# Optimization experiments

Hardware: AMD Instinct MI355X
Metric: run time of the kernel (lower is better)

## Reference

```python
import jax, jax.numpy as jnp
import numpy as np

NUM_NODES = 100000
NUM_EDGES = 1600000
INPUT_DIM = 128
HIDDEN_DIM = 64
OUTPUT_DIM = 2
DROPOUT_P = 0.5


def setup_inputs() -> dict:
    key = jax.random.key(0)
    ks = jax.random.split(key, 6)
    x = jax.random.normal(ks[0], (NUM_NODES, INPUT_DIM), dtype=jnp.float32)
    edge_index = jax.random.randint(ks[1], (2, NUM_EDGES), 0, NUM_NODES, dtype=jnp.int64)
    W_conv = jax.random.normal(ks[2], (INPUT_DIM, HIDDEN_DIM), dtype=jnp.float32) * (1.0 / np.sqrt(INPUT_DIM))
    b_conv = jax.random.normal(ks[3], (HIDDEN_DIM,), dtype=jnp.float32) * 0.02
    W_lin = jax.random.normal(ks[4], (HIDDEN_DIM, OUTPUT_DIM), dtype=jnp.float32) * (1.0 / np.sqrt(HIDDEN_DIM))
    b_lin = jax.random.normal(ks[5], (OUTPUT_DIM,), dtype=jnp.float32) * 0.02
    return {"x": x, "edge_index": edge_index, "W_conv": W_conv, "b_conv": b_conv,
            "W_lin": W_lin, "b_lin": b_lin}


def _gcn_conv(x, edge_index, W, b):
    n = x.shape[0]
    # linear transform first (PyG GCNConv)
    h = x @ W  # [N, hidden]
    # add self-loops
    loop = jnp.arange(n, dtype=edge_index.dtype)
    row = jnp.concatenate([edge_index[0], loop])  # source
    col = jnp.concatenate([edge_index[1], loop])  # target
    # symmetric normalization deg^{-1/2} (degree counted on targets, incl. self-loops)
    deg = jax.ops.segment_sum(jnp.ones_like(col, dtype=h.dtype), col, num_segments=n)
    dinv = jnp.where(deg > 0, jax.lax.rsqrt(deg), 0.0)
    norm = dinv[row] * dinv[col]  # [E+N]
    # gather -> scale -> scatter-add
    msgs = h[row] * norm[:, None]  # [E+N, hidden]
    out = jax.ops.segment_sum(msgs, col, num_segments=n)
    return out + b


def reference(x, edge_index, W_conv, b_conv, W_lin, b_lin):
    h = _gcn_conv(x, edge_index, W_conv, b_conv)
    h = jax.nn.relu(h)
    # dropout p=0.5, training mode, deterministic key for reproducibility
    keep = jax.random.bernoulli(jax.random.key(42), 1.0 - DROPOUT_P, h.shape)
    h = jnp.where(keep, h / (1.0 - DROPOUT_P), 0.0)
    return h @ W_lin + b_lin
```

## Files before the change

### kernel.cpp

```cpp
#include <hip/hip_runtime.h>
#include <hip/hip_bf16.h>

#define N_NODES 100000
#define N_EDGES 1600000
#define IN_DIM 128
#define HID 64
#define NB ((N_NODES + 255) / 256)
#define EPB 4096
#define BUCKET_BLOCKS ((N_EDGES + EPB - 1) / EPB)
#define MAXPB 8192

__device__ __forceinline__ unsigned rotl32(unsigned x, unsigned r) {
    return (x << r) | (x >> (32u - r));
}

__device__ __forceinline__ void threefry2x32_k42(unsigned x0, unsigned x1,
                                                 unsigned& o0, unsigned& o1) {
    const unsigned ks0 = 0u;
    const unsigned ks1 = 42u;
    const unsigned ks2 = 0u ^ 42u ^ 0x1BD11BDAu;
    x0 += ks0; x1 += ks1;
    x0 += x1; x1 = rotl32(x1, 13); x1 ^= x0;
    x0 += x1; x1 = rotl32(x1, 15); x1 ^= x0;
    x0 += x1; x1 = rotl32(x1, 26); x1 ^= x0;
    x0 += x1; x1 = rotl32(x1, 6);  x1 ^= x0;
    x0 += ks1; x1 += ks2 + 1u;
    x0 += x1; x1 = rotl32(x1, 17); x1 ^= x0;
    x0 += x1; x1 = rotl32(x1, 29); x1 ^= x0;
    x0 += x1; x1 = rotl32(x1, 16); x1 ^= x0;
    x0 += x1; x1 = rotl32(x1, 24); x1 ^= x0;
    x0 += ks2; x1 += ks0 + 2u;
    x0 += x1; x1 = rotl32(x1, 13); x1 ^= x0;
    x0 += x1; x1 = rotl32(x1, 15); x1 ^= x0;
    x0 += x1; x1 = rotl32(x1, 26); x1 ^= x0;
    x0 += x1; x1 = rotl32(x1, 6);  x1 ^= x0;
    x0 += ks0; x1 += ks1 + 3u;
    x0 += x1; x1 = rotl32(x1, 17); x1 ^= x0;
    x0 += x1; x1 = rotl32(x1, 29); x1 ^= x0;
    x0 += x1; x1 = rotl32(x1, 16); x1 ^= x0;
    x0 += x1; x1 = rotl32(x1, 24); x1 ^= x0;
    x0 += ks1; x1 += ks2 + 4u;
    x0 += x1; x1 = rotl32(x1, 13); x1 ^= x0;
    x0 += x1; x1 = rotl32(x1, 15); x1 ^= x0;
    x0 += x1; x1 = rotl32(x1, 26); x1 ^= x0;
    x0 += x1; x1 = rotl32(x1, 6);  x1 ^= x0;
    x0 += ks2; x1 += ks0 + 5u;
    o0 = x0; o1 = x1;
}

__device__ __forceinline__ float bf2f(unsigned short u) {
    return __uint_as_float((unsigned)u << 16);
}
__device__ __forceinline__ float bf2f_lo(unsigned u) {
    return __uint_as_float(u << 16);
}
__device__ __forceinline__ float bf2f_hi(unsigned u) {
    return __uint_as_float(u & 0xffff0000u);
}

__global__ __launch_bounds__(512) void k_bucket(const int* __restrict__ src,
                                                const int* __restrict__ dst,
                                                int* __restrict__ bucketcnt,
                                                unsigned* __restrict__ gbuf) {
    __shared__ int cnt[512];
    __shared__ int off[512];
    __shared__ int cur[NB];
    __shared__ int gbase[NB];
    __shared__ unsigned buf[EPB];
    __shared__ unsigned short bkt[EPB];
    const int t = threadIdx.x;
    const int e0 = blockIdx.x * EPB;
    const int n = min(EPB, N_EDGES - e0);
    cnt[t] = 0;
    __syncthreads();
    unsigned myrec[EPB / 512];
    int myb[EPB / 512];
#pragma unroll
    for (int k = 0; k < EPB / 512; k++) {
        int e = e0 + k * 512 + t;
        if (e < N_EDGES) {
            int r = src[e];
            int c = dst[e];
            int b = c >> 8;
            myrec[k] = ((unsigned)(c & 255) << 17) | (unsigned)r;
            myb[k] = b;
            atomicAdd(&cnt[b], 1);
        } else {
            myb[k] = -1;
        }
    }
    __syncthreads();
    int own = cnt[t];
    for (int o = 1; o < 512; o <<= 1) {
        int v = (t >= o) ? cnt[t - o] : 0;
        __syncthreads();
        cnt[t] += v;
        __syncthreads();
    }
    off[t] = cnt[t] - own;
    if (t < NB) {
        cur[t] = off[t];
        gbase[t] = t * MAXPB + (own ? atomicAdd(&bucketcnt[t], own) : 0);
    }
    __syncthreads();
#pragma unroll
    for (int k = 0; k < EPB / 512; k++) {
        if (myb[k] >= 0) {
            int p = atomicAdd(&cur[myb[k]], 1);
            buf[p] = myrec[k];
            bkt[p] = (unsigned short)myb[k];
        }
    }
    __syncthreads();
    for (int j = t; j < n; j += 512) {
        int b = bkt[j];
        gbuf[gbase[b] + (j - off[b])] = buf[j];
    }
}

__global__ __launch_bounds__(512) void k_scanB(const int* __restrict__ bucketcnt,
                                               int* __restrict__ bucket_base) {
    __shared__ int s[512];
    int t = threadIdx.x;
    int own = (t < NB) ? bucketcnt[t] : 0;
    s[t] = own;
    __syncthreads();
    for (int o = 1; o < 512; o <<= 1) {
        int v = (t >= o) ? s[t - o] : 0;
        __syncthreads();
        s[t] += v;
        __syncthreads();
    }
    if (t < NB) bucket_base[t] = s[t] - own;
    if (t == 511) bucket_base[NB] = s[511];
}

__global__ __launch_bounds__(256) void k_csr2(const unsigned* __restrict__ gbuf,
                                              const int* __restrict__ bucketcnt,
                                              const int* __restrict__ bucket_base,
                                              int* __restrict__ row_start,
                                              float* __restrict__ dinv,
                                              int* __restrict__ srcs) {
    __shared__ unsigned lbuf[MAXPB];
    __shared__ int lcnt[256];
    __shared__ int pre[256];
    __shared__ int cur[256];
    const int b = blockIdx.x, t = threadIdx.x;
    const int n = bucketcnt[b];
    const unsigned* reg = gbuf + (size_t)b * MAXPB;
    lcnt[t] = 0;
    for (int j = t; j < n; j += 256) lbuf[j] = reg[j];
    __syncthreads();
    for (int j = t; j < n; j += 256) atomicAdd(&lcnt[lbuf[j] >> 17], 1);
    __syncthreads();
    int my = lcnt[t];
    pre[t] = my;
    __syncthreads();
    for (int o = 1; o < 256; o <<= 1) {
        int v = (t >= o) ? pre[t - o] : 0;
        __syncthreads();
        pre[t] += v;
        __syncthreads();
    }
    const int gb = bucket_base[b];
    int base = gb + pre[t] - my;
    cur[t] = base;
    const int c = b * 256 + t;
    if (c < N_NODES) {
        row_start[c] = base;
        dinv[c] = rsqrtf((float)(my + 1));
    }
    if (b == NB - 1 && t == 255) row_start[N_NODES] = gb + pre[255];
    __syncthreads();
    for (int j = t; j < n; j += 256) {
        unsigned rec = lbuf[j];
        int pos = atomicAdd(&cur[rec >> 17], 1);
        srcs[pos] = (int)(rec & 0x1FFFF);
    }
}

__global__ __launch_bounds__(256) void k_gemm(const float* __restrict__ x,
                                              const float* __restrict__ W,
                                              const float* __restrict__ dinv,
                                              unsigned short* __restrict__ gm) {
    __shared__ float Wl[IN_DIM * HID];
    __shared__ float xs[16][IN_DIM];
    const int t = threadIdx.x;
    const float4* W4 = (const float4*)W;
    for (int i = t; i < IN_DIM * HID / 4; i += 256) ((float4*)Wl)[i] = W4[i];
    const int base = blockIdx.x * 16;
    const float4* x4 = (const float4*)(x + (size_t)base * IN_DIM);
    for (int i = t; i < 16 * IN_DIM / 4; i += 256) ((float4*)xs)[i] = x4[i];
    __syncthreads();
    const int d = t & 63, g = t >> 6;
    float wreg[IN_DIM];
#pragma unroll
    for (int k = 0; k < IN_DIM; k++) wreg[k] = Wl[k * HID + d];
    float a0 = 0.f, a1 = 0.f, a2 = 0.f, a3 = 0.f;
#pragma unroll
    for (int k = 0; k < IN_DIM; k += 4) {
        float4 xv0 = *(const float4*)&xs[g][k];
        float4 xv1 = *(const float4*)&xs[g + 4][k];
        float4 xv2 = *(const float4*)&xs[g + 8][k];
        float4 xv3 = *(const float4*)&xs[g + 12][k];
        a0 += xv0.x * wreg[k] + xv0.y * wreg[k + 1] + xv0.z * wreg[k + 2] + xv0.w * wreg[k + 3];
        a1 += xv1.x * wreg[k] + xv1.y * wreg[k + 1] + xv1.z * wreg[k + 2] + xv1.w * wreg[k + 3];
        a2 += xv2.x * wreg[k] + xv2.y * wreg[k + 1] + xv2.z * wreg[k + 2] + xv2.w * wreg[k + 3];
        a3 += xv3.x * wreg[k] + xv3.y * wreg[k + 1] + xv3.z * wreg[k + 2] + xv3.w * wreg[k + 3];
    }
    a0 *= dinv[base + g];
    a1 *= dinv[base + g + 4];
    a2 *= dinv[base + g + 8];
    a3 *= dinv[base + g + 12];
    gm[(size_t)(base + g) * HID + d]      = __bfloat16_as_ushort(__float2bfloat16(a0));
    gm[(size_t)(base + g + 4) * HID + d]  = __bfloat16_as_ushort(__float2bfloat16(a1));
    gm[(size_t)(base + g + 8) * HID + d]  = __bfloat16_as_ushort(__float2bfloat16(a2));
    gm[(size_t)(base + g + 12) * HID + d] = __bfloat16_as_ushort(__float2bfloat16(a3));
}

__global__ __launch_bounds__(256, 4) void k_aggr(const unsigned short* __restrict__ gm,
                                                 const int* __restrict__ row_start,
                                                 const int* __restrict__ srcs,
                                                 const float* __restrict__ dinv,
                                                 const float* __restrict__ bconv,
                                                 const float* __restrict__ Wlin,
                                                 const float* __restrict__ blin,
                                                 float* __restrict__ out) {
    const int c  = blockIdx.x * 16 + (threadIdx.x >> 4);
    const int d4 = threadIdx.x & 15;
    const int beg = row_start[c];
    const int end = row_start[c + 1];

    const uint2 s0 = *(const uint2*)(gm + ((size_t)c << 6) + (d4 << 2));
    float a0 = bf2f_lo(s0.x), a1 = bf2f_hi(s0.x);
    float a2 = bf2f_lo(s0.y), a3 = bf2f_hi(s0.y);

    int j = beg;
    if (j + 8 <= end) {
        int r[8];
#pragma unroll
        for (int u = 0; u < 8; u++) r[u] = srcs[j + u];
        while (true) {
            uint2 w[8];
#pragma unroll
            for (int u = 0; u < 8; u++)
                w[u] = *(const uint2*)(gm + ((size_t)r[u] << 6) + (d4 << 2));
            j += 8;
            const bool more = (j + 8 <= end);
            int r2[8];
            if (more) {
#pragma unroll
                for (int u = 0; u < 8; u++) r2[u] = srcs[j + u];
            }
#pragma unroll
            for (int u = 0; u < 8; u++) {
                a0 += bf2f_lo(w[u].x); a1 += bf2f_hi(w[u].x);
                a2 += bf2f_lo(w[u].y); a3 += bf2f_hi(w[u].y);
            }
            if (!more) break;
#pragma unroll
            for (int u = 0; u < 8; u++) r[u] = r2[u];
        }
    }
    for (; j < end; j++) {
        const int r = srcs[j];
        const uint2 w = *(const uint2*)(gm + ((size_t)r << 6) + (d4 << 2));
        a0 += bf2f_lo(w.x); a1 += bf2f_hi(w.x);
        a2 += bf2f_lo(w.y); a3 += bf2f_hi(w.y);
    }

    const float dv = dinv[c];
    const float4 bc4 = *(const float4*)(bconv + (d4 << 2));
    float v0 = fmaxf(a0 * dv + bc4.x, 0.f);
    float v1 = fmaxf(a1 * dv + bc4.y, 0.f);
    float v2 = fmaxf(a2 * dv + bc4.z, 0.f);
    float v3 = fmaxf(a3 * dv + bc4.w, 0.f);

    const unsigned ib = (unsigned)(c * HID + (d4 << 2));
    unsigned o0, o1;
    threefry2x32_k42(0u, ib + 0u, o0, o1);
    v0 = ((o0 ^ o1) & 0x80000000u) ? 0.f : v0 * 2.f;
    threefry2x32_k42(0u, ib + 1u, o0, o1);
    v1 = ((o0 ^ o1) & 0x80000000u) ? 0.f : v1 * 2.f;
    threefry2x32_k42(0u, ib + 2u, o0, o1);
    v2 = ((o0 ^ o1) & 0x80000000u) ? 0.f : v2 * 2.f;
    threefry2x32_k42(0u, ib + 3u, o0, o1);
    v3 = ((o0 ^ o1) & 0x80000000u) ? 0.f : v3 * 2.f;

    const float4 wl0 = *(const float4*)(Wlin + (d4 << 3));
    const float4 wl1 = *(const float4*)(Wlin + (d4 << 3) + 4);
    float p0 = v0 * wl0.x + v1 * wl0.z + v2 * wl1.x + v3 * wl1.z;
    float p1 = v0 * wl0.y + v1 * wl0.w + v2 * wl1.y + v3 * wl1.w;

#pragma unroll
    for (int off = 8; off; off >>= 1) {
        p0 += __shfl_xor(p0, off);
        p1 += __shfl_xor(p1, off);
    }
    if (d4 == 0) {
        *(float2*)(out + (size_t)c * 2) = make_float2(p0 + blin[0], p1 + blin[1]);
    }
}

extern "C" void kernel_launch(void* const* d_in, const int* in_sizes, int n_in,
                              void* d_out, int out_size, void* d_ws, size_t ws_size,
                              hipStream_t stream) {
    const float* x  = (const float*)d_in[0];
    const void*  ei = d_in[1];
    const float* Wc = (const float*)d_in[2];
    const float* bc = (const float*)d_in[3];
    const float* Wl = (const float*)d_in[4];
    const float* bl = (const float*)d_in[5];
    for (int i = 0; i < n_in; i++) {
        switch (in_sizes[i]) {
            case N_NODES * IN_DIM:   x  = (const float*)d_in[i]; break;
            case 2 * N_EDGES:
            case 4 * N_EDGES:        ei = d_in[i]; break;
            case IN_DIM * HID:       Wc = (const float*)d_in[i]; break;
            case HID:                bc = (const float*)d_in[i]; break;
            case HID * 2:            Wl = (const float*)d_in[i]; break;
            case 2:                  bl = (const float*)d_in[i]; break;
            default: break;
        }
    }
    float* out = (float*)d_out;

    const int* src = (const int*)ei;
    const int* dst = (const int*)ei + N_EDGES;

    char* ws = (char*)d_ws;
    size_t off = 0;
    unsigned short* gm    = (unsigned short*)(ws + off); off += (size_t)N_NODES * HID * 2;
    float*    dinv        = (float*)(ws + off);    off += (size_t)N_NODES * 4;
    int*      row_start   = (int*)(ws + off);      off += (size_t)(N_NODES + 4) * 4;
    int*      bucketcnt   = (int*)(ws + off);      off += (size_t)(NB + 4) * 4;
    int*      bucket_base = (int*)(ws + off);      off += (size_t)(NB + 4) * 4;
    unsigned* gbuf        = (unsigned*)(ws + off); off += (size_t)NB * MAXPB * 4;
    int*      srcs        = (int*)(ws + off);      off += (size_t)N_EDGES * 4;

    hipMemsetAsync(bucketcnt, 0, (size_t)NB * 4, stream);
    k_bucket<<<BUCKET_BLOCKS, 512, 0, stream>>>(src, dst, bucketcnt, gbuf);
    k_scanB<<<1, 512, 0, stream>>>(bucketcnt, bucket_base);
    k_csr2<<<NB, 256, 0, stream>>>(gbuf, bucketcnt, bucket_base, row_start, dinv, srcs);
    k_gemm<<<N_NODES / 16, 256, 0, stream>>>(x, Wc, dinv, gm);
    k_aggr<<<(N_NODES + 15) / 16, 256, 0, stream>>>(gm, row_start, srcs, dinv, bc, Wl, bl, out);
}
```

Measured before the change: 209.9 us.

## Use bf16 MFMA with hi/lo split for the feature transform GEMM

Replaces the scalar FP32 x@W kernel with a matrix-core version. Both x and W are split into bf16 high and low parts, and three MFMA products (hh, lh, hl) recover near-FP32 accuracy. Each block now covers 64 rows instead of 16, which cuts the number of times W is loaded into shared memory. The cost is conversion overhead, and the output writes are scattered per element, which may not coalesce well.

```diff
diff --git a/kernel.cpp b/kernel.cpp
--- a/kernel.cpp
+++ b/kernel.cpp
@@ -9,6 +9,9 @@
 #define EPB 4096
 #define BUCKET_BLOCKS ((N_EDGES + EPB - 1) / EPB)
 #define MAXPB 8192
+
+typedef __attribute__((ext_vector_type(8))) short bf16x8;
+typedef __attribute__((ext_vector_type(4))) float f32x4;
 
 __device__ __forceinline__ unsigned rotl32(unsigned x, unsigned r) {
     return (x << r) | (x >> (32u - r));
@@ -183,39 +186,87 @@
                                               const float* __restrict__ W,
                                               const float* __restrict__ dinv,
                                               unsigned short* __restrict__ gm) {
-    __shared__ float Wl[IN_DIM * HID];
-    __shared__ float xs[16][IN_DIM];
+    __shared__ unsigned short WtH[HID][136];
+    __shared__ unsigned short WtL[HID][136];
     const int t = threadIdx.x;
-    const float4* W4 = (const float4*)W;
-    for (int i = t; i < IN_DIM * HID / 4; i += 256) ((float4*)Wl)[i] = W4[i];
-    const int base = blockIdx.x * 16;
-    const float4* x4 = (const float4*)(x + (size_t)base * IN_DIM);
-    for (int i = t; i < 16 * IN_DIM / 4; i += 256) ((float4*)xs)[i] = x4[i];
-    __syncthreads();
-    const int d = t & 63, g = t >> 6;
-    float wreg[IN_DIM];
-#pragma unroll
-    for (int k = 0; k < IN_DIM; k++) wreg[k] = Wl[k * HID + d];
-    float a0 = 0.f, a1 = 0.f, a2 = 0.f, a3 = 0.f;
-#pragma unroll
-    for (int k = 0; k < IN_DIM; k += 4) {
-        float4 xv0 = *(const float4*)&xs[g][k];
-        float4 xv1 = *(const float4*)&xs[g + 4][k];
-        float4 xv2 = *(const float4*)&xs[g + 8][k];
-        float4 xv3 = *(const float4*)&xs[g + 12][k];
-        a0 += xv0.x * wreg[k] + xv0.y * wreg[k + 1] + xv0.z * wreg[k + 2] + xv0.w * wreg[k + 3];
-        a1 += xv1.x * wreg[k] + xv1.y * wreg[k + 1] + xv1.z * wreg[k + 2] + xv1.w * wreg[k + 3];
-        a2 += xv2.x * wreg[k] + xv2.y * wreg[k + 1] + xv2.z * wreg[k + 2] + xv2.w * wreg[k + 3];
-        a3 += xv3.x * wreg[k] + xv3.y * wreg[k + 1] + xv3.z * wreg[k + 2] + xv3.w * wreg[k + 3];
-    }
-    a0 *= dinv[base + g];
-    a1 *= dinv[base + g + 4];
-    a2 *= dinv[base + g + 8];
-    a3 *= dinv[base + g + 12];
-    gm[(size_t)(base + g) * HID + d]      = __bfloat16_as_ushort(__float2bfloat16(a0));
-    gm[(size_t)(base + g + 4) * HID + d]  = __bfloat16_as_ushort(__float2bfloat16(a1));
-    gm[(size_t)(base + g + 8) * HID + d]  = __bfloat16_as_ushort(__float2bfloat16(a2));
-    gm[(size_t)(base + g + 12) * HID + d] = __bfloat16_as_ushort(__float2bfloat16(a3));
+    {
+        const int n = t & 63;
+        const int k0 = (t >> 6) * 32;
+        for (int k = k0; k < k0 + 32; k += 2) {
+            float w0 = W[(size_t)k * HID + n];
+            float w1 = W[(size_t)(k + 1) * HID + n];
+            unsigned short h0 = __bfloat16_as_ushort(__float2bfloat16(w0));
+            unsigned short h1 = __bfloat16_as_ushort(__float2bfloat16(w1));
+            unsigned short l0 = __bfloat16_as_ushort(__float2bfloat16(w0 - bf2f(h0)));
+            unsigned short l1 = __bfloat16_as_ushort(__float2bfloat16(w1 - bf2f(h1)));
+            *(unsigned*)&WtH[n][k] = (unsigned)h0 | ((unsigned)h1 << 16);
+            *(unsigned*)&WtL[n][k] = (unsigned)l0 | ((unsigned)l1 << 16);
+        }
+    }
+    __syncthreads();
+
+    const int wave = t >> 6, lane = t & 63;
+    const int row16 = lane & 15;
+    const int kgrp = lane >> 4;
+    const int browA = blockIdx.x * 64 + wave * 16;
+
+    const int rA = min(browA + row16, N_NODES - 1);
+    const float* xr = x + (size_t)rA * IN_DIM + kgrp * 8;
+    float xv[32];
+#pragma unroll
+    for (int ks = 0; ks < 4; ks++) {
+        *(f32x4*)&xv[ks * 8]     = *(const f32x4*)(xr + ks * 32);
+        *(f32x4*)&xv[ks * 8 + 4] = *(const f32x4*)(xr + ks * 32 + 4);
+    }
+    bf16x8 ah[4], al[4];
+#pragma unroll
+    for (int ks = 0; ks < 4; ks++) {
+#pragma unroll
+        for (int j = 0; j < 8; j++) {
+            float v = xv[ks * 8 + j];
+            unsigned short h = __bfloat16_as_ushort(__float2bfloat16(v));
+            unsigned short l = __bfloat16_as_ushort(__float2bfloat16(v - bf2f(h)));
+            ah[ks][j] = (short)h;
+            al[ks][j] = (short)l;
+        }
+    }
+
+    float dv[4];
+    int orow[4];
+#pragma unroll
+    for (int i = 0; i < 4; i++) {
+        orow[i] = browA + kgrp * 4 + i;
+        dv[i] = dinv[min(orow[i], N_NODES - 1)];
+    }
+
+#pragma unroll
+    for (int nt = 0; nt < 4; nt++) {
+        const int n = nt * 16 + row16;
+        bf16x8 bh[4], bl[4];
+#pragma unroll
+        for (int ks = 0; ks < 4; ks++) {
+            bh[ks] = *(const bf16x8*)&WtH[n][ks * 32 + kgrp * 8];
+            bl[ks] = *(const bf16x8*)&WtL[n][ks * 32 + kgrp * 8];
+        }
+        f32x4 acc = {0.f, 0.f, 0.f, 0.f};
+#pragma unroll
+        for (int ks = 0; ks < 4; ks++)
+            acc = __builtin_amdgcn_mfma_f32_16x16x32_bf16(ah[ks], bh[ks], acc, 0, 0, 0);
+#pragma unroll
+        for (int ks = 0; ks < 4; ks++)
+            acc = __builtin_amdgcn_mfma_f32_16x16x32_bf16(al[ks], bh[ks], acc, 0, 0, 0);
+#pragma unroll
+        for (int ks = 0; ks < 4; ks++)
+            acc = __builtin_amdgcn_mfma_f32_16x16x32_bf16(ah[ks], bl[ks], acc, 0, 0, 0);
+#pragma unroll
+        for (int i = 0; i < 4; i++) {
+            if (orow[i] < N_NODES) {
+                float g = acc[i] * dv[i];
+                gm[(size_t)orow[i] * HID + nt * 16 + row16] =
+                    __bfloat16_as_ushort(__float2bfloat16(g));
+            }
+        }
+    }
 }
 
 __global__ __launch_bounds__(256, 4) void k_aggr(const unsigned short* __restrict__ gm,
@@ -342,6 +393,6 @@
     k_bucket<<<BUCKET_BLOCKS, 512, 0, stream>>>(src, dst, bucketcnt, gbuf);
     k_scanB<<<1, 512, 0, stream>>>(bucketcnt, bucket_base);
     k_csr2<<<NB, 256, 0, stream>>>(gbuf, bucketcnt, bucket_base, row_start, dinv, srcs);
-    k_gemm<<<N_NODES / 16, 256, 0, stream>>>(x, Wc, dinv, gm);
+    k_gemm<<<(N_NODES + 63) / 64, 256, 0, stream>>>(x, Wc, dinv, gm);
     k_aggr<<<(N_NODES + 15) / 16, 256, 0, stream>>>(gm, row_start, srcs, dinv, bc, Wl, bl, out);
 }
```

Result: faster. 183.8 us (-12.4%).
